# Optimization experiments

Hardware: AMD Instinct MI355X
Metric: run time of the kernel (lower is better)

## Reference

```python
import jax, jax.numpy as jnp
import numpy as np

WINDOW = 11
K1, K2, L, EPS = 0.01, 0.03, 1.0, 1e-8


def _box_filter(x, window):
    # Depthwise normalized box filter, VALID padding. x: (B, C, H, W)
    c = x.shape[1]
    k = jnp.ones((c, 1, window, window), dtype=x.dtype) / (window * window)
    return jax.lax.conv_general_dilated(
        x, k, window_strides=(1, 1), padding='VALID',
        dimension_numbers=('NCHW', 'OIHW', 'NCHW'),
        feature_group_count=c)


def setup_inputs() -> dict:
    key = jax.random.key(0)
    kx, ky = jax.random.split(key)
    shape = (16, 3, 512, 512)
    x = jax.random.uniform(kx, shape, dtype=jnp.float32)
    y = jax.random.uniform(ky, shape, dtype=jnp.float32)
    return {"x": x, "y": y}


def reference(x, y):
    C1 = (K1 * L) ** 2
    C2 = (K2 * L) ** 2
    mu_x = _box_filter(x, WINDOW)
    mu_y = _box_filter(y, WINDOW)
    mu_x_sq = mu_x * mu_x
    mu_y_sq = mu_y * mu_y
    mu_xy = mu_x * mu_y
    sigma_x_sq = jnp.maximum(_box_filter(x * x, WINDOW) - mu_x_sq, 0.0)
    sigma_y_sq = jnp.maximum(_box_filter(y * y, WINDOW) - mu_y_sq, 0.0)
    sigma_xy = _box_filter(x * y, WINDOW) - mu_xy
    num = (2.0 * mu_xy + C1) * (2.0 * sigma_xy + C2)
    den = (mu_x_sq + mu_y_sq + C1) * (sigma_x_sq + sigma_y_sq + C2) + EPS
    ssim = jnp.mean(num / den)
    return 1.0 - ssim
```

## Files before the change

kernel.cpp:

```cpp
#include <hip/hip_runtime.h>


#define WIN     11
#define IMG     512
#define OUTW    502
#define SEG     16
#define NSEG    32
#define NPLANES 48
#define NPART   (NSEG * NPLANES)
#define HSTR    516

#define C1f     (0.01f * 0.01f)
#define C2f     (0.03f * 0.03f)
#define EPSf    1e-8f
#define INV121  (1.0f / 121.0f)

__global__ __launch_bounds__(64) void ssim_zero(double* acc) {
    if (threadIdx.x == 0) acc[0] = 0.0;
}

__global__ __launch_bounds__(128) void ssim_main(const float* __restrict__ x,
                                                 const float* __restrict__ y,
                                                 double* __restrict__ part,
                                                 int mode) {
    __shared__ float H[2][5][HSTR];
    __shared__ float wsum[2];

    const int t     = threadIdx.x;
    const int plane = blockIdx.y;
    const int seg   = blockIdx.x;
    const int o0    = seg * SEG;
    const int o1    = (o0 + SEG < OUTW) ? (o0 + SEG) : OUTW;
    const int r0    = o0;
    const int r1    = o1 + WIN - 2;

    const float4* xp4 = (const float4*)(x + (size_t)plane * IMG * IMG);
    const float4* yp4 = (const float4*)(y + (size_t)plane * IMG * IMG);

    const int  c0     = 4 * t;
    const bool active = (c0 < OUTW);

    if (t < 4) {
#pragma unroll
        for (int b = 0; b < 2; ++b)
#pragma unroll
            for (int q = 0; q < 5; ++q)
                H[b][q][512 + t] = 0.0f;
    }

    float Vx[4]  = {0.f, 0.f, 0.f, 0.f};
    float Vy[4]  = {0.f, 0.f, 0.f, 0.f};
    float Vxx[4] = {0.f, 0.f, 0.f, 0.f};
    float Vyy[4] = {0.f, 0.f, 0.f, 0.f};
    float Vxy[4] = {0.f, 0.f, 0.f, 0.f};

    float4 nx = xp4[r0 * 128 + t];
    float4 ny = yp4[r0 * 128 + t];
    float4 ox = make_float4(0.f, 0.f, 0.f, 0.f);
    float4 oy = make_float4(0.f, 0.f, 0.f, 0.f);

    float lsum = 0.0f;
    int buf = 0;

    for (int r = r0; r <= r1; ++r) {
        float4 nx2 = nx, ny2 = ny, ox2 = ox, oy2 = oy;
        if (r < r1) {
            nx2 = xp4[(r + 1) * 128 + t];
            ny2 = yp4[(r + 1) * 128 + t];
            if (r - r0 >= WIN - 1) {
                ox2 = xp4[(r + 1 - WIN) * 128 + t];
                oy2 = yp4[(r + 1 - WIN) * 128 + t];
            }
        }

        if (r - r0 >= WIN) {
            const float xo[4] = {ox.x, ox.y, ox.z, ox.w};
            const float yo[4] = {oy.x, oy.y, oy.z, oy.w};
#pragma unroll
            for (int j = 0; j < 4; ++j) {
                Vx[j] -= xo[j];
                Vy[j] -= yo[j];
                Vxx[j] = fmaf(-xo[j], xo[j], Vxx[j]);
                Vyy[j] = fmaf(-yo[j], yo[j], Vyy[j]);
                Vxy[j] = fmaf(-xo[j], yo[j], Vxy[j]);
            }
        }
        {
            const float xn[4] = {nx.x, nx.y, nx.z, nx.w};
            const float yn[4] = {ny.x, ny.y, ny.z, ny.w};
#pragma unroll
            for (int j = 0; j < 4; ++j) {
                Vx[j] += xn[j];
                Vy[j] += yn[j];
                Vxx[j] = fmaf(xn[j], xn[j], Vxx[j]);
                Vyy[j] = fmaf(yn[j], yn[j], Vyy[j]);
                Vxy[j] = fmaf(xn[j], yn[j], Vxy[j]);
            }
        }

        ((float4*)&H[buf][0][0])[t] = make_float4(Vx[0],  Vx[1],  Vx[2],  Vx[3]);
        ((float4*)&H[buf][1][0])[t] = make_float4(Vy[0],  Vy[1],  Vy[2],  Vy[3]);
        ((float4*)&H[buf][2][0])[t] = make_float4(Vxx[0], Vxx[1], Vxx[2], Vxx[3]);
        ((float4*)&H[buf][3][0])[t] = make_float4(Vyy[0], Vyy[1], Vyy[2], Vyy[3]);
        ((float4*)&H[buf][4][0])[t] = make_float4(Vxy[0], Vxy[1], Vxy[2], Vxy[3]);
        __syncthreads();

        if (active && r - r0 >= WIN - 1) {
            float hx[4], hy[4], hxx[4], hyy[4], hxy[4];
#define HORIZ(V, q, h)                                                        \
            {                                                                 \
                const float4* rp = (const float4*)&H[buf][q][0];              \
                float4 n1 = rp[t + 1], n2 = rp[t + 2], n3 = rp[t + 3];        \
                h[0] = ((V[0] + V[1]) + (V[2] + V[3]))                        \
                     + ((n1.x + n1.y) + (n1.z + n1.w))                        \
                     + ((n2.x + n2.y) + n2.z);                                \
                h[1] = h[0] - V[0] + n2.w;                                    \
                h[2] = h[1] - V[1] + n3.x;                                    \
                h[3] = h[2] - V[2] + n3.y;                                    \
            }
            HORIZ(Vx,  0, hx)
            HORIZ(Vy,  1, hy)
            HORIZ(Vxx, 2, hxx)
            HORIZ(Vyy, 3, hyy)
            HORIZ(Vxy, 4, hxy)
#undef HORIZ
#pragma unroll
            for (int j = 0; j < 4; ++j) {
                if (c0 + j < OUTW) {
                    float mux = hx[j]  * INV121, muy = hy[j]  * INV121;
                    float ex2 = hxx[j] * INV121, ey2 = hyy[j] * INV121;
                    float exy = hxy[j] * INV121;
                    float mxs = mux * mux, mys = muy * muy, mxy = mux * muy;
                    float sx  = fmaxf(fmaf(-mux, mux, ex2), 0.0f);
                    float sy  = fmaxf(fmaf(-muy, muy, ey2), 0.0f);
                    float sxy = exy - mxy;
                    float num = fmaf(2.0f, mxy, C1f) * fmaf(2.0f, sxy, C2f);
                    float den = fmaf(mxs + mys + C1f, sx + sy + C2f, EPSf);
                    float rr  = __builtin_amdgcn_rcpf(den);
                    rr = rr * (2.0f - den * rr);
                    lsum = fmaf(num, rr, lsum);
                }
            }
        }

        buf ^= 1;
        nx = nx2; ny = ny2; ox = ox2; oy = oy2;
    }

#pragma unroll
    for (int off = 32; off > 0; off >>= 1) lsum += __shfl_down(lsum, off, 64);
    const int wid = t >> 6, lane = t & 63;
    if (lane == 0) wsum[wid] = lsum;
    __syncthreads();
    if (t == 0) {
        double bs = (double)(wsum[0] + wsum[1]);
        if (mode == 0) part[blockIdx.y * NSEG + blockIdx.x] = bs;
        else           atomicAdd(part, bs);
    }
}

__global__ __launch_bounds__(256) void ssim_final(const double* __restrict__ part,
                                                  int n, float* __restrict__ out) {
    __shared__ double s[4];
    double v = 0.0;
    for (int i = threadIdx.x; i < n; i += 256) v += part[i];
#pragma unroll
    for (int off = 32; off > 0; off >>= 1) v += __shfl_down(v, off, 64);
    if ((threadIdx.x & 63) == 0) s[threadIdx.x >> 6] = v;
    __syncthreads();
    if (threadIdx.x == 0) {
        double tot = s[0] + s[1] + s[2] + s[3];
        const double N = (double)NPLANES * OUTW * OUTW;
        out[0] = 1.0f - (float)(tot / N);
    }
}

extern "C" void kernel_launch(void* const* d_in, const int* in_sizes, int n_in,
                              void* d_out, int out_size, void* d_ws, size_t ws_size,
                              hipStream_t stream) {
    const float* x = (const float*)d_in[0];
    const float* y = (const float*)d_in[1];
    float* out = (float*)d_out;
    double* part = (double*)d_ws;

    if (ws_size >= (size_t)NPART * sizeof(double)) {
        ssim_main<<<dim3(NSEG, NPLANES), dim3(128), 0, stream>>>(x, y, part, 0);
        ssim_final<<<dim3(1), dim3(256), 0, stream>>>(part, NPART, out);
    } else {
        ssim_zero<<<dim3(1), dim3(64), 0, stream>>>(part);
        ssim_main<<<dim3(NSEG, NPLANES), dim3(128), 0, stream>>>(x, y, part, 1);
        ssim_final<<<dim3(1), dim3(256), 0, stream>>>(part, 1, out);
    }
}
```

Before: 140.4 us.

## Use 256 threads with two columns each and prefetch two rows ahead

Each block now runs 256 threads, each owning two output columns with float2 loads instead of four columns with float4, which doubles the threads per block and the waves in flight. Global row loads are prefetched two iterations ahead instead of one, giving more time to hide latency. The horizontal pass now reads five neighbour float2s per quantity from shared memory, so LDS traffic per output rises. Every thread reads past its own columns up to t+5, so the padding row is dropped. Smaller per-thread state and a launch-bounds hint aim at higher occupancy.

```diff
diff --git a/kernel.cpp b/kernel.cpp
--- a/kernel.cpp
+++ b/kernel.cpp
@@ -8,7 +8,6 @@
 #define NSEG    32
 #define NPLANES 48
 #define NPART   (NSEG * NPLANES)
-#define HSTR    516
 
 #define C1f     (0.01f * 0.01f)
 #define C2f     (0.03f * 0.03f)
@@ -19,12 +18,12 @@
     if (threadIdx.x == 0) acc[0] = 0.0;
 }
 
-__global__ __launch_bounds__(128) void ssim_main(const float* __restrict__ x,
-                                                 const float* __restrict__ y,
-                                                 double* __restrict__ part,
-                                                 int mode) {
-    __shared__ float H[2][5][HSTR];
-    __shared__ float wsum[2];
+__global__ __launch_bounds__(256, 6) void ssim_main(const float* __restrict__ x,
+                                                    const float* __restrict__ y,
+                                                    double* __restrict__ part,
+                                                    int mode) {
+    __shared__ float H[2][5][IMG];
+    __shared__ float wsum[4];
 
     const int t     = threadIdx.x;
     const int plane = blockIdx.y;
@@ -34,50 +33,45 @@
     const int r0    = o0;
     const int r1    = o1 + WIN - 2;
 
-    const float4* xp4 = (const float4*)(x + (size_t)plane * IMG * IMG);
-    const float4* yp4 = (const float4*)(y + (size_t)plane * IMG * IMG);
+    const float2* xp2 = (const float2*)(x + (size_t)plane * IMG * IMG);
+    const float2* yp2 = (const float2*)(y + (size_t)plane * IMG * IMG);
 
-    const int  c0     = 4 * t;
-    const bool active = (c0 < OUTW);
+    const int  c0     = 2 * t;
+    const bool active = (t <= 250);
 
-    if (t < 4) {
-#pragma unroll
-        for (int b = 0; b < 2; ++b)
-#pragma unroll
-            for (int q = 0; q < 5; ++q)
-                H[b][q][512 + t] = 0.0f;
-    }
+    float Vx[2]  = {0.f, 0.f};
+    float Vy[2]  = {0.f, 0.f};
+    float Vxx[2] = {0.f, 0.f};
+    float Vyy[2] = {0.f, 0.f};
+    float Vxy[2] = {0.f, 0.f};
 
-    float Vx[4]  = {0.f, 0.f, 0.f, 0.f};
-    float Vy[4]  = {0.f, 0.f, 0.f, 0.f};
-    float Vxx[4] = {0.f, 0.f, 0.f, 0.f};
-    float Vyy[4] = {0.f, 0.f, 0.f, 0.f};
-    float Vxy[4] = {0.f, 0.f, 0.f, 0.f};
-
-    float4 nx = xp4[r0 * 128 + t];
-    float4 ny = yp4[r0 * 128 + t];
-    float4 ox = make_float4(0.f, 0.f, 0.f, 0.f);
-    float4 oy = make_float4(0.f, 0.f, 0.f, 0.f);
+    const float2 z2 = make_float2(0.f, 0.f);
+    float2 n0x = xp2[(size_t)r0 * 256 + t];
+    float2 n0y = yp2[(size_t)r0 * 256 + t];
+    float2 n1x = xp2[(size_t)(r0 + 1) * 256 + t];
+    float2 n1y = yp2[(size_t)(r0 + 1) * 256 + t];
+    float2 o0x = z2, o0y = z2, o1x = z2, o1y = z2;
 
     float lsum = 0.0f;
     int buf = 0;
 
     for (int r = r0; r <= r1; ++r) {
-        float4 nx2 = nx, ny2 = ny, ox2 = ox, oy2 = oy;
-        if (r < r1) {
-            nx2 = xp4[(r + 1) * 128 + t];
-            ny2 = yp4[(r + 1) * 128 + t];
-            if (r - r0 >= WIN - 1) {
-                ox2 = xp4[(r + 1 - WIN) * 128 + t];
-                oy2 = yp4[(r + 1 - WIN) * 128 + t];
+        float2 nnx = z2, nny = z2, oox = z2, ooy = z2;
+        const int rc = r + 2;
+        if (rc <= r1) {
+            nnx = xp2[(size_t)rc * 256 + t];
+            nny = yp2[(size_t)rc * 256 + t];
+            if (rc - r0 >= WIN) {
+                oox = xp2[(size_t)(rc - WIN) * 256 + t];
+                ooy = yp2[(size_t)(rc - WIN) * 256 + t];
             }
         }
 
         if (r - r0 >= WIN) {
-            const float xo[4] = {ox.x, ox.y, ox.z, ox.w};
-            const float yo[4] = {oy.x, oy.y, oy.z, oy.w};
+            const float xo[2] = {o0x.x, o0x.y};
+            const float yo[2] = {o0y.x, o0y.y};
 #pragma unroll
-            for (int j = 0; j < 4; ++j) {
+            for (int j = 0; j < 2; ++j) {
                 Vx[j] -= xo[j];
                 Vy[j] -= yo[j];
                 Vxx[j] = fmaf(-xo[j], xo[j], Vxx[j]);
@@ -86,10 +80,10 @@
             }
         }
         {
-            const float xn[4] = {nx.x, nx.y, nx.z, nx.w};
-            const float yn[4] = {ny.x, ny.y, ny.z, ny.w};
+            const float xn[2] = {n0x.x, n0x.y};
+            const float yn[2] = {n0y.x, n0y.y};
 #pragma unroll
-            for (int j = 0; j < 4; ++j) {
+            for (int j = 0; j < 2; ++j) {
                 Vx[j] += xn[j];
                 Vy[j] += yn[j];
                 Vxx[j] = fmaf(xn[j], xn[j], Vxx[j]);
@@ -98,38 +92,41 @@
             }
         }
 
-        ((float4*)&H[buf][0][0])[t] = make_float4(Vx[0],  Vx[1],  Vx[2],  Vx[3]);
-        ((float4*)&H[buf][1][0])[t] = make_float4(Vy[0],  Vy[1],  Vy[2],  Vy[3]);
-        ((float4*)&H[buf][2][0])[t] = make_float4(Vxx[0], Vxx[1], Vxx[2], Vxx[3]);
-        ((float4*)&H[buf][3][0])[t] = make_float4(Vyy[0], Vyy[1], Vyy[2], Vyy[3]);
-        ((float4*)&H[buf][4][0])[t] = make_float4(Vxy[0], Vxy[1], Vxy[2], Vxy[3]);
+        ((float2*)&H[buf][0][0])[t] = make_float2(Vx[0],  Vx[1]);
+        ((float2*)&H[buf][1][0])[t] = make_float2(Vy[0],  Vy[1]);
+        ((float2*)&H[buf][2][0])[t] = make_float2(Vxx[0], Vxx[1]);
+        ((float2*)&H[buf][3][0])[t] = make_float2(Vyy[0], Vyy[1]);
+        ((float2*)&H[buf][4][0])[t] = make_float2(Vxy[0], Vxy[1]);
         __syncthreads();
 
         if (active && r - r0 >= WIN - 1) {
-            float hx[4], hy[4], hxx[4], hyy[4], hxy[4];
-#define HORIZ(V, q, h)                                                        \
-            {                                                                 \
-                const float4* rp = (const float4*)&H[buf][q][0];              \
-                float4 n1 = rp[t + 1], n2 = rp[t + 2], n3 = rp[t + 3];        \
-                h[0] = ((V[0] + V[1]) + (V[2] + V[3]))                        \
-                     + ((n1.x + n1.y) + (n1.z + n1.w))                        \
-                     + ((n2.x + n2.y) + n2.z);                                \
-                h[1] = h[0] - V[0] + n2.w;                                    \
-                h[2] = h[1] - V[1] + n3.x;                                    \
-                h[3] = h[2] - V[2] + n3.y;                                    \
+            float h0[5], h1[5];
+#pragma unroll
+            for (int q = 0; q < 5; ++q) {
+                const float2* rp = (const float2*)&H[buf][q][0];
+                float2 m1 = rp[t + 1], m2 = rp[t + 2], m3 = rp[t + 3];
+                float2 m4 = rp[t + 4], m5 = rp[t + 5];
+                float own0, own1;
+                switch (q) {
+                    case 0: own0 = Vx[0];  own1 = Vx[1];  break;
+                    case 1: own0 = Vy[0];  own1 = Vy[1];  break;
+                    case 2: own0 = Vxx[0]; own1 = Vxx[1]; break;
+                    case 3: own0 = Vyy[0]; own1 = Vyy[1]; break;
+                    default:own0 = Vxy[0]; own1 = Vxy[1]; break;
+                }
+                float s = ((own0 + own1) + (m1.x + m1.y))
+                        + ((m2.x + m2.y) + (m3.x + m3.y))
+                        + ((m4.x + m4.y) + m5.x);
+                h0[q] = s;
+                h1[q] = s - own0 + m5.y;
             }
-            HORIZ(Vx,  0, hx)
-            HORIZ(Vy,  1, hy)
-            HORIZ(Vxx, 2, hxx)
-            HORIZ(Vyy, 3, hyy)
-            HORIZ(Vxy, 4, hxy)
-#undef HORIZ
 #pragma unroll
-            for (int j = 0; j < 4; ++j) {
+            for (int j = 0; j < 2; ++j) {
                 if (c0 + j < OUTW) {
-                    float mux = hx[j]  * INV121, muy = hy[j]  * INV121;
-                    float ex2 = hxx[j] * INV121, ey2 = hyy[j] * INV121;
-                    float exy = hxy[j] * INV121;
+                    const float* h = j ? h1 : h0;
+                    float mux = h[0] * INV121, muy = h[1] * INV121;
+                    float ex2 = h[2] * INV121, ey2 = h[3] * INV121;
+                    float exy = h[4] * INV121;
                     float mxs = mux * mux, mys = muy * muy, mxy = mux * muy;
                     float sx  = fmaxf(fmaf(-mux, mux, ex2), 0.0f);
                     float sy  = fmaxf(fmaf(-muy, muy, ey2), 0.0f);
@@ -144,7 +141,8 @@
         }
 
         buf ^= 1;
-        nx = nx2; ny = ny2; ox = ox2; oy = oy2;
+        n0x = n1x; n1x = nnx;  n0y = n1y; n1y = nny;
+        o0x = o1x; o1x = oox;  o0y = o1y; o1y = ooy;
     }
 
 #pragma unroll
@@ -153,7 +151,7 @@
     if (lane == 0) wsum[wid] = lsum;
     __syncthreads();
     if (t == 0) {
-        double bs = (double)(wsum[0] + wsum[1]);
+        double bs = (double)((wsum[0] + wsum[1]) + (wsum[2] + wsum[3]));
         if (mode == 0) part[blockIdx.y * NSEG + blockIdx.x] = bs;
         else           atomicAdd(part, bs);
     }
@@ -169,7 +167,7 @@
     if ((threadIdx.x & 63) == 0) s[threadIdx.x >> 6] = v;
     __syncthreads();
     if (threadIdx.x == 0) {
-        double tot = s[0] + s[1] + s[2] + s[3];
+        double tot = (s[0] + s[1]) + (s[2] + s[3]);
         const double N = (double)NPLANES * OUTW * OUTW;
         out[0] = 1.0f - (float)(tot / N);
     }
@@ -184,11 +182,11 @@
     double* part = (double*)d_ws;
 
     if (ws_size >= (size_t)NPART * sizeof(double)) {
-        ssim_main<<<dim3(NSEG, NPLANES), dim3(128), 0, stream>>>(x, y, part, 0);
+        ssim_main<<<dim3(NSEG, NPLANES), dim3(256), 0, stream>>>(x, y, part, 0);
         ssim_final<<<dim3(1), dim3(256), 0, stream>>>(part, NPART, out);
     } else {
         ssim_zero<<<dim3(1), dim3(64), 0, stream>>>(part);
-        ssim_main<<<dim3(NSEG, NPLANES), dim3(128), 0, stream>>>(x, y, part, 1);
+        ssim_main<<<dim3(NSEG, NPLANES), dim3(256), 0, stream>>>(x, y, part, 1);
         ssim_final<<<dim3(1), dim3(256), 0, stream>>>(part, 1, out);
     }
 }
```

Result: slower. 143.7 us (+2.4%).

## Use single-wave blocks with 8 columns per lane and wave-level barriers

Applied to the files above, without the earlier changes.

Each block becomes one 64-lane wave, with each lane handling 8 columns. This lets the horizontal pass use only wave barriers instead of block-wide __syncthreads, and the LDS buffer is no longer double-buffered. Row segments shrink from 16 to 8 rows, which doubles the block count for more parallelism but adds more redundant window rows per segment. The SSIM arithmetic is rescaled to work on raw sums with constants multiplied by 121 and 121^2, which removes the per-value divisions.

```diff
diff --git a/kernel.cpp b/kernel.cpp
--- a/kernel.cpp
+++ b/kernel.cpp
@@ -3,81 +3,96 @@
 
 #define WIN     11
 #define IMG     512
+#define PLSZ    (IMG * IMG)
 #define OUTW    502
-#define SEG     16
-#define NSEG    32
+#define SEG     8
+#define NSEG    63
 #define NPLANES 48
 #define NPART   (NSEG * NPLANES)
-#define HSTR    516
-
-#define C1f     (0.01f * 0.01f)
-#define C2f     (0.03f * 0.03f)
-#define EPSf    1e-8f
-#define INV121  (1.0f / 121.0f)
+
+#define C1S   1.4641f
+#define C2S   13.1769f
+#define EPS4  2.1434881f
 
 __global__ __launch_bounds__(64) void ssim_zero(double* acc) {
     if (threadIdx.x == 0) acc[0] = 0.0;
 }
 
-__global__ __launch_bounds__(128) void ssim_main(const float* __restrict__ x,
-                                                 const float* __restrict__ y,
-                                                 double* __restrict__ part,
-                                                 int mode) {
-    __shared__ float H[2][5][HSTR];
-    __shared__ float wsum[2];
-
-    const int t     = threadIdx.x;
+__global__ __launch_bounds__(64) void ssim_main(const float* __restrict__ x,
+                                                const float* __restrict__ y,
+                                                double* __restrict__ part,
+                                                int mode) {
+    __shared__ __align__(16) float H[5][2][264];
+
+    const int lane  = threadIdx.x;
+    const int seg   = blockIdx.x;
     const int plane = blockIdx.y;
-    const int seg   = blockIdx.x;
     const int o0    = seg * SEG;
     const int o1    = (o0 + SEG < OUTW) ? (o0 + SEG) : OUTW;
     const int r0    = o0;
     const int r1    = o1 + WIN - 2;
-
-    const float4* xp4 = (const float4*)(x + (size_t)plane * IMG * IMG);
-    const float4* yp4 = (const float4*)(y + (size_t)plane * IMG * IMG);
-
-    const int  c0     = 4 * t;
-    const bool active = (c0 < OUTW);
-
-    if (t < 4) {
-#pragma unroll
-        for (int b = 0; b < 2; ++b)
-#pragma unroll
-            for (int q = 0; q < 5; ++q)
-                H[b][q][512 + t] = 0.0f;
-    }
-
-    float Vx[4]  = {0.f, 0.f, 0.f, 0.f};
-    float Vy[4]  = {0.f, 0.f, 0.f, 0.f};
-    float Vxx[4] = {0.f, 0.f, 0.f, 0.f};
-    float Vyy[4] = {0.f, 0.f, 0.f, 0.f};
-    float Vxy[4] = {0.f, 0.f, 0.f, 0.f};
-
-    float4 nx = xp4[r0 * 128 + t];
-    float4 ny = yp4[r0 * 128 + t];
-    float4 ox = make_float4(0.f, 0.f, 0.f, 0.f);
-    float4 oy = make_float4(0.f, 0.f, 0.f, 0.f);
-
-    float lsum = 0.0f;
-    int buf = 0;
+    const int c0    = 8 * lane;
+
+    if (lane < 20) {
+        const int q = lane >> 2, rem = lane & 3;
+        *(float4*)&H[q][rem >> 1][256 + ((rem & 1) << 2)] =
+            make_float4(0.f, 0.f, 0.f, 0.f);
+    }
+
+    const float* xp = x + plane * PLSZ;
+    const float* yp = y + plane * PLSZ;
+
+    float Vx[8]  = {0,0,0,0,0,0,0,0};
+    float Vy[8]  = {0,0,0,0,0,0,0,0};
+    float Vxx[8] = {0,0,0,0,0,0,0,0};
+    float Vyy[8] = {0,0,0,0,0,0,0,0};
+    float Vxy[8] = {0,0,0,0,0,0,0,0};
+
+    const float4 z4 = make_float4(0.f, 0.f, 0.f, 0.f);
+    float4 nx0, nx1, ny0, ny1;
+    float4 nX0 = z4, nX1 = z4, nY0 = z4, nY1 = z4;
+    float4 ox0 = z4, ox1 = z4, oy0 = z4, oy1 = z4;
+    float4 oX0 = z4, oX1 = z4, oY0 = z4, oY1 = z4;
+
+    {
+        const float4* px = (const float4*)(xp + r0 * IMG + c0);
+        const float4* py = (const float4*)(yp + r0 * IMG + c0);
+        nx0 = px[0]; nx1 = px[1]; ny0 = py[0]; ny1 = py[1];
+    }
+
+    float lsum = 0.f;
 
     for (int r = r0; r <= r1; ++r) {
-        float4 nx2 = nx, ny2 = ny, ox2 = ox, oy2 = oy;
-        if (r < r1) {
-            nx2 = xp4[(r + 1) * 128 + t];
-            ny2 = yp4[(r + 1) * 128 + t];
-            if (r - r0 >= WIN - 1) {
-                ox2 = xp4[(r + 1 - WIN) * 128 + t];
-                oy2 = yp4[(r + 1 - WIN) * 128 + t];
-            }
-        }
-
+        const int rn = r + 1;
+        if (rn <= r1) {
+            const float4* px = (const float4*)(xp + rn * IMG + c0);
+            const float4* py = (const float4*)(yp + rn * IMG + c0);
+            nX0 = px[0]; nX1 = px[1]; nY0 = py[0]; nY1 = py[1];
+            const int ro = rn - WIN;
+            if (ro >= r0) {
+                const float4* qx = (const float4*)(xp + ro * IMG + c0);
+                const float4* qy = (const float4*)(yp + ro * IMG + c0);
+                oX0 = qx[0]; oX1 = qx[1]; oY0 = qy[0]; oY1 = qy[1];
+            }
+        }
+
+        {
+            const float xn[8] = {nx0.x,nx0.y,nx0.z,nx0.w, nx1.x,nx1.y,nx1.z,nx1.w};
+            const float yn[8] = {ny0.x,ny0.y,ny0.z,ny0.w, ny1.x,ny1.y,ny1.z,ny1.w};
+#pragma unroll
+            for (int j = 0; j < 8; ++j) {
+                Vx[j] += xn[j];
+                Vy[j] += yn[j];
+                Vxx[j] = fmaf(xn[j], xn[j], Vxx[j]);
+                Vyy[j] = fmaf(yn[j], yn[j], Vyy[j]);
+                Vxy[j] = fmaf(xn[j], yn[j], Vxy[j]);
+            }
+        }
         if (r - r0 >= WIN) {
-            const float xo[4] = {ox.x, ox.y, ox.z, ox.w};
-            const float yo[4] = {oy.x, oy.y, oy.z, oy.w};
-#pragma unroll
-            for (int j = 0; j < 4; ++j) {
+            const float xo[8] = {ox0.x,ox0.y,ox0.z,ox0.w, ox1.x,ox1.y,ox1.z,ox1.w};
+            const float yo[8] = {oy0.x,oy0.y,oy0.z,oy0.w, oy1.x,oy1.y,oy1.z,oy1.w};
+#pragma unroll
+            for (int j = 0; j < 8; ++j) {
                 Vx[j] -= xo[j];
                 Vy[j] -= yo[j];
                 Vxx[j] = fmaf(-xo[j], xo[j], Vxx[j]);
@@ -85,77 +100,75 @@
                 Vxy[j] = fmaf(-xo[j], yo[j], Vxy[j]);
             }
         }
-        {
-            const float xn[4] = {nx.x, nx.y, nx.z, nx.w};
-            const float yn[4] = {ny.x, ny.y, ny.z, ny.w};
-#pragma unroll
-            for (int j = 0; j < 4; ++j) {
-                Vx[j] += xn[j];
-                Vy[j] += yn[j];
-                Vxx[j] = fmaf(xn[j], xn[j], Vxx[j]);
-                Vyy[j] = fmaf(yn[j], yn[j], Vyy[j]);
-                Vxy[j] = fmaf(xn[j], yn[j], Vxy[j]);
-            }
-        }
-
-        ((float4*)&H[buf][0][0])[t] = make_float4(Vx[0],  Vx[1],  Vx[2],  Vx[3]);
-        ((float4*)&H[buf][1][0])[t] = make_float4(Vy[0],  Vy[1],  Vy[2],  Vy[3]);
-        ((float4*)&H[buf][2][0])[t] = make_float4(Vxx[0], Vxx[1], Vxx[2], Vxx[3]);
-        ((float4*)&H[buf][3][0])[t] = make_float4(Vyy[0], Vyy[1], Vyy[2], Vyy[3]);
-        ((float4*)&H[buf][4][0])[t] = make_float4(Vxy[0], Vxy[1], Vxy[2], Vxy[3]);
-        __syncthreads();
-
-        if (active && r - r0 >= WIN - 1) {
-            float hx[4], hy[4], hxx[4], hyy[4], hxy[4];
-#define HORIZ(V, q, h)                                                        \
-            {                                                                 \
-                const float4* rp = (const float4*)&H[buf][q][0];              \
-                float4 n1 = rp[t + 1], n2 = rp[t + 2], n3 = rp[t + 3];        \
-                h[0] = ((V[0] + V[1]) + (V[2] + V[3]))                        \
-                     + ((n1.x + n1.y) + (n1.z + n1.w))                        \
-                     + ((n2.x + n2.y) + n2.z);                                \
-                h[1] = h[0] - V[0] + n2.w;                                    \
-                h[2] = h[1] - V[1] + n3.x;                                    \
-                h[3] = h[2] - V[2] + n3.y;                                    \
-            }
-            HORIZ(Vx,  0, hx)
-            HORIZ(Vy,  1, hy)
-            HORIZ(Vxx, 2, hxx)
-            HORIZ(Vyy, 3, hyy)
-            HORIZ(Vxy, 4, hxy)
+
+        if (r - r0 >= WIN - 1) {
+            __builtin_amdgcn_wave_barrier();
+            ((float4*)&H[0][0][4 * lane])[0] = make_float4(Vx[0],  Vx[1],  Vx[2],  Vx[3]);
+            ((float4*)&H[0][1][4 * lane])[0] = make_float4(Vx[4],  Vx[5],  Vx[6],  Vx[7]);
+            ((float4*)&H[1][0][4 * lane])[0] = make_float4(Vy[0],  Vy[1],  Vy[2],  Vy[3]);
+            ((float4*)&H[1][1][4 * lane])[0] = make_float4(Vy[4],  Vy[5],  Vy[6],  Vy[7]);
+            ((float4*)&H[2][0][4 * lane])[0] = make_float4(Vxx[0], Vxx[1], Vxx[2], Vxx[3]);
+            ((float4*)&H[2][1][4 * lane])[0] = make_float4(Vxx[4], Vxx[5], Vxx[6], Vxx[7]);
+            ((float4*)&H[3][0][4 * lane])[0] = make_float4(Vyy[0], Vyy[1], Vyy[2], Vyy[3]);
+            ((float4*)&H[3][1][4 * lane])[0] = make_float4(Vyy[4], Vyy[5], Vyy[6], Vyy[7]);
+            ((float4*)&H[4][0][4 * lane])[0] = make_float4(Vxy[0], Vxy[1], Vxy[2], Vxy[3]);
+            ((float4*)&H[4][1][4 * lane])[0] = make_float4(Vxy[4], Vxy[5], Vxy[6], Vxy[7]);
+            __builtin_amdgcn_wave_barrier();
+
+            float h[5][8];
+#define HORIZ(Q, VA)                                                           \
+            {                                                                  \
+                const float4 lo1 = *(const float4*)&H[Q][0][4 * lane + 4];     \
+                const float4 hi1 = *(const float4*)&H[Q][1][4 * lane + 4];     \
+                const float4 lo2 = *(const float4*)&H[Q][0][4 * lane + 8];     \
+                float s = ((VA[0] + VA[1]) + (VA[2] + VA[3]))                  \
+                        + ((VA[4] + VA[5]) + (VA[6] + VA[7]));                 \
+                s += (lo1.x + lo1.y) + lo1.z;                                  \
+                h[Q][0] = s;                                                   \
+                s += lo1.w - VA[0]; h[Q][1] = s;                               \
+                s += hi1.x - VA[1]; h[Q][2] = s;                               \
+                s += hi1.y - VA[2]; h[Q][3] = s;                               \
+                s += hi1.z - VA[3]; h[Q][4] = s;                               \
+                s += hi1.w - VA[4]; h[Q][5] = s;                               \
+                s += lo2.x - VA[5]; h[Q][6] = s;                               \
+                s += lo2.y - VA[6]; h[Q][7] = s;                               \
+            }
+            HORIZ(0, Vx)
+            HORIZ(1, Vy)
+            HORIZ(2, Vxx)
+            HORIZ(3, Vyy)
+            HORIZ(4, Vxy)
 #undef HORIZ
-#pragma unroll
-            for (int j = 0; j < 4; ++j) {
+
+#pragma unroll
+            for (int j = 0; j < 8; ++j) {
                 if (c0 + j < OUTW) {
-                    float mux = hx[j]  * INV121, muy = hy[j]  * INV121;
-                    float ex2 = hxx[j] * INV121, ey2 = hyy[j] * INV121;
-                    float exy = hxy[j] * INV121;
-                    float mxs = mux * mux, mys = muy * muy, mxy = mux * muy;
-                    float sx  = fmaxf(fmaf(-mux, mux, ex2), 0.0f);
-                    float sy  = fmaxf(fmaf(-muy, muy, ey2), 0.0f);
-                    float sxy = exy - mxy;
-                    float num = fmaf(2.0f, mxy, C1f) * fmaf(2.0f, sxy, C2f);
-                    float den = fmaf(mxs + mys + C1f, sx + sy + C2f, EPSf);
-                    float rr  = __builtin_amdgcn_rcpf(den);
-                    rr = rr * (2.0f - den * rr);
-                    lsum = fmaf(num, rr, lsum);
+                    const float X  = h[0][j], Y  = h[1][j];
+                    const float XX = h[2][j], YY = h[3][j], XY = h[4][j];
+                    const float x2 = X * X, y2 = Y * Y, xy = X * Y;
+                    const float A  = fmaf(2.f, xy, C1S);
+                    const float B  = fmaf(2.f, fmaf(121.f, XY, -xy), C2S);
+                    const float Cc = x2 + y2 + C1S;
+                    const float sx = fmaxf(fmaf(121.f, XX, -x2), 0.f);
+                    const float sy = fmaxf(fmaf(121.f, YY, -y2), 0.f);
+                    const float D  = (sx + sy) + C2S;
+                    const float den = fmaf(Cc, D, EPS4);
+                    float rr = __builtin_amdgcn_rcpf(den);
+                    rr = rr * (2.f - den * rr);
+                    lsum = fmaf(A * B, rr, lsum);
                 }
             }
         }
 
-        buf ^= 1;
-        nx = nx2; ny = ny2; ox = ox2; oy = oy2;
+        nx0 = nX0; nx1 = nX1; ny0 = nY0; ny1 = nY1;
+        ox0 = oX0; ox1 = oX1; oy0 = oY0; oy1 = oY1;
     }
 
 #pragma unroll
     for (int off = 32; off > 0; off >>= 1) lsum += __shfl_down(lsum, off, 64);
-    const int wid = t >> 6, lane = t & 63;
-    if (lane == 0) wsum[wid] = lsum;
-    __syncthreads();
-    if (t == 0) {
-        double bs = (double)(wsum[0] + wsum[1]);
-        if (mode == 0) part[blockIdx.y * NSEG + blockIdx.x] = bs;
-        else           atomicAdd(part, bs);
+    if (lane == 0) {
+        if (mode == 0) part[plane * NSEG + seg] = (double)lsum;
+        else           atomicAdd(part, (double)lsum);
     }
 }
 
@@ -169,7 +182,7 @@
     if ((threadIdx.x & 63) == 0) s[threadIdx.x >> 6] = v;
     __syncthreads();
     if (threadIdx.x == 0) {
-        double tot = s[0] + s[1] + s[2] + s[3];
+        double tot = (s[0] + s[1]) + (s[2] + s[3]);
         const double N = (double)NPLANES * OUTW * OUTW;
         out[0] = 1.0f - (float)(tot / N);
     }
@@ -184,11 +197,11 @@
     double* part = (double*)d_ws;
 
     if (ws_size >= (size_t)NPART * sizeof(double)) {
-        ssim_main<<<dim3(NSEG, NPLANES), dim3(128), 0, stream>>>(x, y, part, 0);
+        ssim_main<<<dim3(NSEG, NPLANES), dim3(64), 0, stream>>>(x, y, part, 0);
         ssim_final<<<dim3(1), dim3(256), 0, stream>>>(part, NPART, out);
     } else {
         ssim_zero<<<dim3(1), dim3(64), 0, stream>>>(part);
-        ssim_main<<<dim3(NSEG, NPLANES), dim3(128), 0, stream>>>(x, y, part, 1);
+        ssim_main<<<dim3(NSEG, NPLANES), dim3(64), 0, stream>>>(x, y, part, 1);
         ssim_final<<<dim3(1), dim3(256), 0, stream>>>(part, 1, out);
     }
 }
```

Result: slower. 150.0 us (+6.8%).
